# Performance work log

Measured on AMD Instinct MI355X. Metric: run time of the kernel, lower is better.

## Reference

```python
import jax, jax.numpy as jnp
import numpy as np

B, S, D, H = 2, 2048, 1024, 16
DK = D // H  # 64


def setup_inputs() -> dict:
    key = jax.random.key(0)
    ks = jax.random.split(key, 4)
    scale = 1.0 / np.sqrt(D)
    return {
        "q_input": jax.random.normal(ks[0], (B, S, D), dtype=jnp.float32),
        "W_q": jax.random.normal(ks[1], (D, D), dtype=jnp.float32) * scale,
        "b_q": jnp.zeros((D,), dtype=jnp.float32),
        "W_k": jax.random.normal(ks[2], (D, D), dtype=jnp.float32) * scale,
        "b_k": jnp.zeros((D,), dtype=jnp.float32),
        "W_v": jax.random.normal(ks[3], (D, D), dtype=jnp.float32) * scale,
        "b_v": jnp.zeros((D,), dtype=jnp.float32),
    }


def reference(q_input, W_q, b_q, W_k, b_k, W_v, b_v):
    # Self-attention: k_input and v_input default to q_input in the torch module.
    # nn.Linear computes x @ W.T + b
    q = q_input @ W_q.T + b_q
    k = q_input @ W_k.T + b_k
    v = q_input @ W_v.T + b_v

    # [B,S,D] -> [B,H,S,DK]
    def split_heads(x):
        return x.reshape(B, S, H, DK).transpose(0, 2, 1, 3)

    qh, kh, vh = split_heads(q), split_heads(k), split_heads(v)

    # scores [B,H,S,S]; causal mask added BEFORE scaling (as in source; -inf invariant)
    scores = jnp.einsum("bhqd,bhkd->bhqk", qh, kh)
    causal = jnp.tril(jnp.ones((S, S), dtype=bool))
    scores = jnp.where(causal[None, None], scores, -jnp.inf)
    scores = scores / jnp.sqrt(jnp.float32(DK))
    probs = jax.nn.softmax(scores, axis=-1)
    z = jnp.einsum("bhqk,bhkd->bhqd", probs, vh)  # [B,H,S,DK]
    # [B,H,S,DK] -> [B,S,H,DK] -> [B,S,D]
    return z.transpose(0, 2, 1, 3).reshape(B, S, D)
```

## Files before the change

### kernel.cpp

```cpp
#include <hip/hip_runtime.h>
#include <hip/hip_bf16.h>
#include <stdint.h>

typedef __attribute__((ext_vector_type(8))) short short8;
typedef __attribute__((ext_vector_type(4))) short short4v;
typedef __attribute__((ext_vector_type(4))) float f32x4;

#define B_ 2
#define S_ 2048
#define D_ 1024
#define H_ 16
#define DK_ 64
#define M_ (B_*S_)

#define WS_QKV   0
#define WS_XB    12582912
#define WS_WB    16777216

#define QSCALE (0.125f * 1.44269504088896f)

#define GLL16(g, l) __builtin_amdgcn_global_load_lds( \
    (const __attribute__((address_space(1))) void*)(g), \
    (__attribute__((address_space(3))) void*)(l), 16, 0, 0)

#define WAIT_VM0 asm volatile("s_waitcnt vmcnt(0)" ::: "memory")
#define WAIT_VM4 asm volatile("s_waitcnt vmcnt(4)" ::: "memory")
#define BARRIER_RAW asm volatile("s_barrier" ::: "memory")

static __device__ __forceinline__ short f2bf(float f){
  union { float f; unsigned u; } x; x.f = f;
  unsigned r = x.u + 0x7fff + ((x.u >> 16) & 1);
  return (short)(r >> 16);
}

__global__ __launch_bounds__(256) void cvt_bf16(
    const float* __restrict__ X,  const float* __restrict__ Wq,
    const float* __restrict__ Wk, const float* __restrict__ Wv,
    short* __restrict__ ws)
{
  const int z = blockIdx.z;
  const float* src; short* dst; int n;
  if (z == 0)      { src = X;  dst = ws + WS_XB;               n = M_*D_; }
  else if (z == 1) { src = Wq; dst = ws + WS_WB;               n = D_*D_; }
  else if (z == 2) { src = Wk; dst = ws + WS_WB + D_*D_;       n = D_*D_; }
  else             { src = Wv; dst = ws + WS_WB + 2*(D_*D_);   n = D_*D_; }
  const int stride = gridDim.x * blockDim.x * 4;
  for (int i = (blockIdx.x * blockDim.x + threadIdx.x) * 4; i < n; i += stride) {
    float4 v = *(const float4*)(src + i);
    short4v o;
    o.x = f2bf(v.x); o.y = f2bf(v.y); o.z = f2bf(v.z); o.w = f2bf(v.w);
    *(short4v*)(dst + i) = o;
  }
}

__global__ __launch_bounds__(256, 3) void qkv_gemm(
    const short* __restrict__ ws_in,
    const float* __restrict__ bq, const float* __restrict__ bk,
    const float* __restrict__ bv, short* __restrict__ qkv)
{
  const int z = blockIdx.z;
  const short* X  = ws_in + WS_XB;
  const short* Wm = ws_in + WS_WB + (size_t)z * (D_*D_);
  const float* bias = (z==0) ? bq : (z==1) ? bk : bv;
  short* out = qkv + (size_t)z * (M_*D_);

  __shared__ short lds[24576];

  const int t = threadIdx.x;
  const int w = t >> 6, lane = t & 63;
  const int quad = lane >> 4, l16 = lane & 15;
  const int wm = w & 1, wn = w >> 1;
  const int m0 = blockIdx.y * 128, n0 = blockIdx.x * 128;

  const int lr = lane >> 2, lc = lane & 3;
  const int csrc = lc ^ (lr & 3);
  const size_t arow0 = (size_t)(m0 + w*16     + lr) * D_ + csrc*8;
  const size_t arow1 = (size_t)(m0 + (w+4)*16 + lr) * D_ + csrc*8;
  const size_t brow0 = (size_t)(n0 + w*16     + lr) * D_ + csrc*8;
  const size_t brow1 = (size_t)(n0 + (w+4)*16 + lr) * D_ + csrc*8;

  f32x4 acc[4][4];
  #pragma unroll
  for (int i=0;i<4;i++)
    #pragma unroll
    for (int j=0;j<4;j++) acc[i][j] = (f32x4){0.f,0.f,0.f,0.f};

  #pragma unroll
  for (int p=0;p<2;p++){
    GLL16(X  + arow0 + p*32, lds + p*4096 + (w*16)*32);
    GLL16(X  + arow1 + p*32, lds + p*4096 + ((w+4)*16)*32);
    GLL16(Wm + brow0 + p*32, lds + 12288 + p*4096 + (w*16)*32);
    GLL16(Wm + brow1 + p*32, lds + 12288 + p*4096 + ((w+4)*16)*32);
  }

  const int ca = quad ^ (l16 & 3);
  int cur = 0;
  for (int kk = 0; kk < 32; kk++) {
    if (kk < 31) { WAIT_VM4; }
    else         { WAIT_VM0; }
    BARRIER_RAW;
    if (kk < 30) {
      int slot = cur + 2; if (slot >= 3) slot -= 3;
      const int ko = (kk+2)*32;
      short* An = lds + slot*4096;
      short* Bn = lds + 12288 + slot*4096;
      GLL16(X  + arow0 + ko, An + (w*16)*32);
      GLL16(X  + arow1 + ko, An + ((w+4)*16)*32);
      GLL16(Wm + brow0 + ko, Bn + (w*16)*32);
      GLL16(Wm + brow1 + ko, Bn + ((w+4)*16)*32);
    }
    const short* Ac = lds + cur*4096;
    const short* Bc = lds + 12288 + cur*4096;
    short8 af[4], bfr[4];
    #pragma unroll
    for (int mt=0;mt<4;mt++)
      af[mt] = *(const short8*)(Ac + (wm*64 + mt*16 + l16)*32 + ca*8);
    #pragma unroll
    for (int nt=0;nt<4;nt++)
      bfr[nt] = *(const short8*)(Bc + (wn*64 + nt*16 + l16)*32 + ca*8);
    if (z != 2) {
      #pragma unroll
      for (int mt=0;mt<4;mt++)
        #pragma unroll
        for (int nt=0;nt<4;nt++)
          acc[mt][nt] = __builtin_amdgcn_mfma_f32_16x16x32_bf16(af[mt], bfr[nt], acc[mt][nt], 0,0,0);
    } else {
      #pragma unroll
      for (int nt=0;nt<4;nt++)
        #pragma unroll
        for (int mt=0;mt<4;mt++)
          acc[nt][mt] = __builtin_amdgcn_mfma_f32_16x16x32_bf16(bfr[nt], af[mt], acc[nt][mt], 0,0,0);
    }
    cur = (cur==2) ? 0 : cur+1;
  }

  __syncthreads();

  if (z != 2) {
    const float scale = (z==0) ? QSCALE : 1.0f;
    #pragma unroll
    for (int nt=0;nt<4;nt++){
      const int col_l = wn*64 + nt*16 + l16;
      const float bvv = bias[n0 + col_l];
      #pragma unroll
      for (int mt=0;mt<4;mt++)
        #pragma unroll
        for (int i=0;i<4;i++){
          const int row_l = wm*64 + mt*16 + quad*4 + i;
          lds[row_l*136 + col_l] = f2bf((acc[mt][nt][i] + bvv) * scale);
        }
    }
    __syncthreads();
    #pragma unroll
    for (int k=0;k<8;k++){
      const int cid = k*256 + t;
      const int row = cid >> 4, cc = cid & 15;
      short8 vv = *(const short8*)(lds + row*136 + cc*8);
      const int m = m0 + row, bidx = m >> 11, s = m & 2047;
      const int n = n0 + cc*8, h = n >> 6, dd = n & 63;
      *(short8*)(out + (((size_t)(bidx*H_ + h))*S_ + s)*DK_ + dd) = vv;
    }
  } else {
    #pragma unroll
    for (int nt=0;nt<4;nt++)
      #pragma unroll
      for (int i=0;i<4;i++){
        const int n_l = wn*64 + nt*16 + quad*4 + i;
        const float bvv = bias[n0 + n_l];
        #pragma unroll
        for (int mt=0;mt<4;mt++){
          const int m_l = wm*64 + mt*16 + l16;
          lds[n_l*136 + m_l] = f2bf(acc[nt][mt][i] + bvv);
        }
      }
    __syncthreads();
    #pragma unroll
    for (int k=0;k<8;k++){
      const int cid = k*256 + t;
      const int rowN = cid >> 4, cc = cid & 15;
      short8 vv = *(const short8*)(lds + rowN*136 + cc*8);
      const int n = n0 + rowN, h = n >> 6, dd = n & 63;
      const int m = m0 + cc*8, bidx = m >> 11, s0 = m & 2047;
      *(short8*)(out + (((size_t)(bidx*H_ + h))*DK_ + dd)*S_ + s0) = vv;
    }
  }
}

__global__ __launch_bounds__(256, 3) void attn(
    const short* __restrict__ qkv, float* __restrict__ out)
{
  const int bh = blockIdx.y;
  const int qt = (gridDim.x - 1) - blockIdx.x;
  const short* Q  = qkv + (size_t)bh * (S_*DK_);
  const short* K  = Q + (size_t)(M_*D_);
  const short* VT = qkv + (size_t)(2*M_*D_) + (size_t)bh * (DK_*S_);

  __shared__ short Kbuf[2][4096];
  __shared__ short Vbuf[2][4096];
  __shared__ short Ps[8192];

  const int t = threadIdx.x;
  const int w = t >> 6, lane = t & 63;
  const int quad = lane >> 4, l16 = lane & 15;
  const int sw = l16 & 7;
  const int lr = lane >> 3, lc = lane & 7;
  const int csrc = lc ^ lr;

  short8 bq[2][2];
  #pragma unroll
  for (int kc=0;kc<2;kc++)
    #pragma unroll
    for (int mt=0;mt<2;mt++)
      bq[kc][mt] = *(const short8*)(Q + (size_t)(qt*128 + w*32 + mt*16 + l16)*DK_
                                      + (kc*4 + quad)*8);

  const int nkt = 2*qt + 2;
  #pragma unroll
  for (int j=0;j<2;j++){
    const int rb = (j*4 + w)*8;
    GLL16(K  + (size_t)(rb + lr)*DK_ + csrc*8, &Kbuf[0][0] + rb*64);
    GLL16(VT + (size_t)(rb + lr)*S_  + csrc*8, &Vbuf[0][0] + rb*64);
  }

  f32x4 o[2][4];
  float lsum[2];
  #pragma unroll
  for (int mt=0;mt<2;mt++){
    #pragma unroll
    for (int nd=0;nd<4;nd++) o[mt][nd] = (f32x4){0.f,0.f,0.f,0.f};
    lsum[mt] = 0.f;
  }

  const int pw_half = (quad & 1) * 4;
  const int pw_ckb  = quad >> 1;
  int cur = 0;

  for (int kt = 0; kt < nkt; kt++){
    WAIT_VM0;
    BARRIER_RAW;
    const int nxt = cur ^ 1;
    if (kt + 1 < nkt) {
      const int kb2 = (kt+1)*64;
      short* Kn = &Kbuf[nxt][0];
      short* Vn = &Vbuf[nxt][0];
      #pragma unroll
      for (int j=0;j<2;j++){
        const int rb = (j*4 + w)*8;
        GLL16(K  + (size_t)(kb2 + rb + lr)*DK_ + csrc*8, Kn + rb*64);
        GLL16(VT + (size_t)(rb + lr)*S_ + kb2 + csrc*8,  Vn + rb*64);
      }
    }
    const short* Kc = &Kbuf[cur][0];
    const short* Vc = &Vbuf[cur][0];
    const int kb = kt*64;

    f32x4 sc[4][2];
    #pragma unroll
    for (int ntk=0;ntk<4;ntk++)
      #pragma unroll
      for (int mt=0;mt<2;mt++) sc[ntk][mt] = (f32x4){0.f,0.f,0.f,0.f};
    #pragma unroll
    for (int kc=0;kc<2;kc++){
      const int xch = (kc*4 + quad) ^ sw;
      short8 ak[4];
      #pragma unroll
      for (int ntk=0;ntk<4;ntk++)
        ak[ntk] = *(const short8*)(Kc + (ntk*16 + l16)*64 + xch*8);
      #pragma unroll
      for (int ntk=0;ntk<4;ntk++)
        #pragma unroll
        for (int mt=0;mt<2;mt++)
          sc[ntk][mt] = __builtin_amdgcn_mfma_f32_16x16x32_bf16(ak[ntk], bq[kc][mt], sc[ntk][mt], 0,0,0);
    }

    const int q0w = qt*128 + w*32;
    if (kb + 63 > q0w) {
      #pragma unroll
      for (int ntk=0;ntk<4;ntk++)
        #pragma unroll
        for (int mt=0;mt<2;mt++){
          const int qg = q0w + mt*16 + l16;
          #pragma unroll
          for (int i=0;i<4;i++){
            const int kg = kb + ntk*16 + quad*4 + i;
            if (kg > qg) sc[ntk][mt][i] = -3.0e38f;
          }
        }
    }

    #pragma unroll
    for (int mt=0;mt<2;mt++){
      const int r = w*32 + mt*16 + l16;
      #pragma unroll
      for (int ntk=0;ntk<4;ntk++){
        float p0 = __builtin_amdgcn_exp2f(sc[ntk][mt][0]);
        float p1 = __builtin_amdgcn_exp2f(sc[ntk][mt][1]);
        float p2 = __builtin_amdgcn_exp2f(sc[ntk][mt][2]);
        float p3 = __builtin_amdgcn_exp2f(sc[ntk][mt][3]);
        lsum[mt] += (p0+p1) + (p2+p3);
        unsigned lo = __builtin_amdgcn_perm(__float_as_uint(p1), __float_as_uint(p0), 0x07060302u);
        unsigned hi = __builtin_amdgcn_perm(__float_as_uint(p3), __float_as_uint(p2), 0x07060302u);
        const int slot = (ntk*2 + pw_ckb) ^ sw;
        *(uint2*)(Ps + r*64 + slot*8 + pw_half) = make_uint2(lo, hi);
      }
    }
    asm volatile("" ::: "memory");

    #pragma unroll
    for (int kc=0;kc<2;kc++){
      const int xch = (kc*4 + quad) ^ sw;
      short8 pa[2], vb[4];
      #pragma unroll
      for (int mt=0;mt<2;mt++)
        pa[mt] = *(const short8*)(Ps + (w*32 + mt*16 + l16)*64 + xch*8);
      #pragma unroll
      for (int nd=0;nd<4;nd++)
        vb[nd] = *(const short8*)(Vc + (nd*16 + l16)*64 + xch*8);
      #pragma unroll
      for (int mt=0;mt<2;mt++)
        #pragma unroll
        for (int nd=0;nd<4;nd++)
          o[mt][nd] = __builtin_amdgcn_mfma_f32_16x16x32_bf16(pa[mt], vb[nd], o[mt][nd], 0,0,0);
    }
    cur = nxt;
  }

  const int bb = bh >> 4, h = bh & 15;
  float linv[2];
  #pragma unroll
  for (int mt=0;mt<2;mt++){
    float rs = lsum[mt];
    rs += __shfl_xor(rs, 16, 64);
    rs += __shfl_xor(rs, 32, 64);
    linv[mt] = 1.0f / rs;
  }
  #pragma unroll
  for (int mt=0;mt<2;mt++){
    #pragma unroll
    for (int i=0;i<4;i++){
      const float lw = __shfl(linv[mt], (quad<<4) + (quad<<2) + i, 64);
      const int q = qt*128 + w*32 + mt*16 + quad*4 + i;
      #pragma unroll
      for (int nd=0;nd<4;nd++){
        const int d = nd*16 + l16;
        out[ ((size_t)bb*S_ + q)*D_ + h*DK_ + d ] = o[mt][nd][i] * lw;
      }
    }
  }
}

extern "C" void kernel_launch(void* const* d_in, const int* in_sizes, int n_in,
                              void* d_out, int out_size, void* d_ws, size_t ws_size,
                              hipStream_t stream)
{
  (void)in_sizes; (void)n_in; (void)out_size; (void)ws_size;
  const float* X  = (const float*)d_in[0];
  const float* Wq = (const float*)d_in[1];
  const float* bq = (const float*)d_in[2];
  const float* Wk = (const float*)d_in[3];
  const float* bk = (const float*)d_in[4];
  const float* Wv = (const float*)d_in[5];
  const float* bv = (const float*)d_in[6];
  short* ws  = (short*)d_ws;
  float* out = (float*)d_out;

  dim3 g0(1024, 1, 4);
  cvt_bf16<<<g0, dim3(256,1,1), 0, stream>>>(X, Wq, Wk, Wv, ws);
  dim3 g1(D_/128, M_/128, 3);
  qkv_gemm<<<g1, dim3(256,1,1), 0, stream>>>(ws, bq, bk, bv, ws + WS_QKV);
  dim3 g2(S_/128, B_*H_);
  attn<<<g2, dim3(256,1,1), 0, stream>>>(ws + WS_QKV, out);
}
```

Baseline: 181.5 us.

## Enlarge QKV GEMM to 256x256 tiles with 8 waves and 4-stage LDS pipeline

The QKV projection GEMM moves from 128x128 tiles with 4 waves and a 3-slot buffer to 256x256 tiles with 8 waves, a 4-slot LDS ring, and a split-phase schedule that interleaves A/B global-to-LDS loads between two MFMA halves, raising s_setprio around the MFMA blocks. The aim is more data reuse per loaded byte and better overlap of loads with matrix math. The epilogue is rewritten to stage half the tile at a time through LDS. In exchange, the grid shrinks to 192 blocks, which may underfill the GPU's CUs, and register and LDS pressure per block rise.

```diff
diff --git a/kernel.cpp b/kernel.cpp
--- a/kernel.cpp
+++ b/kernel.cpp
@@ -25,6 +25,8 @@
 
 #define WAIT_VM0 asm volatile("s_waitcnt vmcnt(0)" ::: "memory")
 #define WAIT_VM4 asm volatile("s_waitcnt vmcnt(4)" ::: "memory")
+#define WAIT_VM8 asm volatile("s_waitcnt vmcnt(8)" ::: "memory")
+#define WAIT_LGKM0 asm volatile("s_waitcnt lgkmcnt(0)" ::: "memory")
 #define BARRIER_RAW asm volatile("s_barrier" ::: "memory")
 
 static __device__ __forceinline__ short f2bf(float f){
@@ -53,7 +55,7 @@
   }
 }
 
-__global__ __launch_bounds__(256, 3) void qkv_gemm(
+__global__ __launch_bounds__(512, 2) void qkv_gemm(
     const short* __restrict__ ws_in,
     const float* __restrict__ bq, const float* __restrict__ bk,
     const float* __restrict__ bv, short* __restrict__ qkv)
@@ -61,127 +63,157 @@
   const int z = blockIdx.z;
   const short* X  = ws_in + WS_XB;
   const short* Wm = ws_in + WS_WB + (size_t)z * (D_*D_);
-  const float* bias = (z==0) ? bq : (z==1) ? bk : bv;
   short* out = qkv + (size_t)z * (M_*D_);
 
-  __shared__ short lds[24576];
+  __shared__ __align__(16) short lds[65536];
 
   const int t = threadIdx.x;
   const int w = t >> 6, lane = t & 63;
   const int quad = lane >> 4, l16 = lane & 15;
-  const int wm = w & 1, wn = w >> 1;
-  const int m0 = blockIdx.y * 128, n0 = blockIdx.x * 128;
-
-  const int lr = lane >> 2, lc = lane & 3;
-  const int csrc = lc ^ (lr & 3);
-  const size_t arow0 = (size_t)(m0 + w*16     + lr) * D_ + csrc*8;
-  const size_t arow1 = (size_t)(m0 + (w+4)*16 + lr) * D_ + csrc*8;
-  const size_t brow0 = (size_t)(n0 + w*16     + lr) * D_ + csrc*8;
-  const size_t brow1 = (size_t)(n0 + (w+4)*16 + lr) * D_ + csrc*8;
-
-  f32x4 acc[4][4];
-  #pragma unroll
-  for (int i=0;i<4;i++)
+  const int wm = w >> 2, wn = w & 3;
+  const int m0 = blockIdx.y * 256, n0 = blockIdx.x * 256;
+
+  const int rl = t >> 2;
+  const int sl = (t & 3) ^ (rl & 3);
+  const short* sA0 = X  + (size_t)(m0 + rl) * D_ + sl*8;
+  const short* sA1 = sA0 + (size_t)128 * D_;
+  const short* sB0 = Wm + (size_t)(n0 + rl) * D_ + sl*8;
+  const short* sB1 = sB0 + (size_t)128 * D_;
+  const int ldsw = w << 9;
+
+  const int swz = quad ^ (l16 & 3);
+
+  f32x4 acc[8][4];
+  #pragma unroll
+  for (int i=0;i<8;i++)
     #pragma unroll
     for (int j=0;j<4;j++) acc[i][j] = (f32x4){0.f,0.f,0.f,0.f};
 
   #pragma unroll
-  for (int p=0;p<2;p++){
-    GLL16(X  + arow0 + p*32, lds + p*4096 + (w*16)*32);
-    GLL16(X  + arow1 + p*32, lds + p*4096 + ((w+4)*16)*32);
-    GLL16(Wm + brow0 + p*32, lds + 12288 + p*4096 + (w*16)*32);
-    GLL16(Wm + brow1 + p*32, lds + 12288 + p*4096 + ((w+4)*16)*32);
-  }
-
-  const int ca = quad ^ (l16 & 3);
-  int cur = 0;
-  for (int kk = 0; kk < 32; kk++) {
-    if (kk < 31) { WAIT_VM4; }
-    else         { WAIT_VM0; }
+  for (int p=0;p<3;p++){
+    GLL16(sA0 + p*32, lds + p*16384 + ldsw);
+    GLL16(sA1 + p*32, lds + p*16384 + 4096 + ldsw);
+    GLL16(sB0 + p*32, lds + p*16384 + 8192 + ldsw);
+    GLL16(sB1 + p*32, lds + p*16384 + 12288 + ldsw);
+  }
+  WAIT_VM8;
+  BARRIER_RAW;
+
+  for (int kt = 0; kt < 32; kt++) {
+    const int bf = kt & 3;
+    const short* bufA = lds + bf*16384;
+    const short* bufB = bufA + 8192;
+    const int tb = (kt + 3) & 3;
+    const int ko2 = (kt + 3) * 32;
+    const bool st = (kt + 3) < 32;
+
+    short8 aF[4], bF[4];
+    #pragma unroll
+    for (int mf=0; mf<4; mf++)
+      aF[mf] = *(const short8*)(bufA + (wm*128 + mf*16 + l16)*32 + swz*8);
+    #pragma unroll
+    for (int nf=0; nf<4; nf++)
+      bF[nf] = *(const short8*)(bufB + (wn*64 + nf*16 + l16)*32 + swz*8);
+    if (st) {
+      GLL16(sA0 + ko2, lds + tb*16384 + ldsw);
+      GLL16(sA1 + ko2, lds + tb*16384 + 4096 + ldsw);
+    }
     BARRIER_RAW;
-    if (kk < 30) {
-      int slot = cur + 2; if (slot >= 3) slot -= 3;
-      const int ko = (kk+2)*32;
-      short* An = lds + slot*4096;
-      short* Bn = lds + 12288 + slot*4096;
-      GLL16(X  + arow0 + ko, An + (w*16)*32);
-      GLL16(X  + arow1 + ko, An + ((w+4)*16)*32);
-      GLL16(Wm + brow0 + ko, Bn + (w*16)*32);
-      GLL16(Wm + brow1 + ko, Bn + ((w+4)*16)*32);
-    }
-    const short* Ac = lds + cur*4096;
-    const short* Bc = lds + 12288 + cur*4096;
-    short8 af[4], bfr[4];
-    #pragma unroll
-    for (int mt=0;mt<4;mt++)
-      af[mt] = *(const short8*)(Ac + (wm*64 + mt*16 + l16)*32 + ca*8);
-    #pragma unroll
-    for (int nt=0;nt<4;nt++)
-      bfr[nt] = *(const short8*)(Bc + (wn*64 + nt*16 + l16)*32 + ca*8);
-    if (z != 2) {
-      #pragma unroll
-      for (int mt=0;mt<4;mt++)
-        #pragma unroll
-        for (int nt=0;nt<4;nt++)
-          acc[mt][nt] = __builtin_amdgcn_mfma_f32_16x16x32_bf16(af[mt], bfr[nt], acc[mt][nt], 0,0,0);
-    } else {
-      #pragma unroll
-      for (int nt=0;nt<4;nt++)
-        #pragma unroll
-        for (int mt=0;mt<4;mt++)
-          acc[nt][mt] = __builtin_amdgcn_mfma_f32_16x16x32_bf16(bfr[nt], af[mt], acc[nt][mt], 0,0,0);
-    }
-    cur = (cur==2) ? 0 : cur+1;
+    WAIT_LGKM0;
+    __builtin_amdgcn_s_setprio(1);
+    #pragma unroll
+    for (int mf=0; mf<4; mf++)
+      #pragma unroll
+      for (int nf=0; nf<4; nf++)
+        acc[mf][nf] = __builtin_amdgcn_mfma_f32_16x16x32_bf16(aF[mf], bF[nf], acc[mf][nf], 0,0,0);
+    __builtin_amdgcn_s_setprio(0);
+    BARRIER_RAW;
+
+    #pragma unroll
+    for (int mf=0; mf<4; mf++)
+      aF[mf] = *(const short8*)(bufA + (wm*128 + 64 + mf*16 + l16)*32 + swz*8);
+    if (st) {
+      GLL16(sB0 + ko2, lds + tb*16384 + 8192 + ldsw);
+      GLL16(sB1 + ko2, lds + tb*16384 + 12288 + ldsw);
+    }
+    BARRIER_RAW;
+    WAIT_LGKM0;
+    __builtin_amdgcn_s_setprio(1);
+    #pragma unroll
+    for (int mf=0; mf<4; mf++)
+      #pragma unroll
+      for (int nf=0; nf<4; nf++)
+        acc[4+mf][nf] = __builtin_amdgcn_mfma_f32_16x16x32_bf16(aF[mf], bF[nf], acc[4+mf][nf], 0,0,0);
+    __builtin_amdgcn_s_setprio(0);
+    if      (kt < 29)  { WAIT_VM8; }
+    else if (kt == 29) { WAIT_VM4; }
+    else if (kt == 30) { WAIT_VM0; }
+    BARRIER_RAW;
   }
 
   __syncthreads();
 
   if (z != 2) {
     const float scale = (z==0) ? QSCALE : 1.0f;
-    #pragma unroll
-    for (int nt=0;nt<4;nt++){
-      const int col_l = wn*64 + nt*16 + l16;
-      const float bvv = bias[n0 + col_l];
-      #pragma unroll
-      for (int mt=0;mt<4;mt++)
+    const float* bias = (z==0) ? bq : bk;
+    float bv4[4];
+    #pragma unroll
+    for (int nf=0; nf<4; nf++) bv4[nf] = bias[n0 + wn*64 + nf*16 + l16];
+    short* ep = lds;
+    #pragma unroll
+    for (int p=0; p<2; p++){
+      if (wm == p){
         #pragma unroll
-        for (int i=0;i<4;i++){
-          const int row_l = wm*64 + mt*16 + quad*4 + i;
-          lds[row_l*136 + col_l] = f2bf((acc[mt][nt][i] + bvv) * scale);
-        }
-    }
-    __syncthreads();
-    #pragma unroll
-    for (int k=0;k<8;k++){
-      const int cid = k*256 + t;
-      const int row = cid >> 4, cc = cid & 15;
-      short8 vv = *(const short8*)(lds + row*136 + cc*8);
-      const int m = m0 + row, bidx = m >> 11, s = m & 2047;
-      const int n = n0 + cc*8, h = n >> 6, dd = n & 63;
-      *(short8*)(out + (((size_t)(bidx*H_ + h))*S_ + s)*DK_ + dd) = vv;
+        for (int mf=0; mf<8; mf++)
+          #pragma unroll
+          for (int nf=0; nf<4; nf++)
+            #pragma unroll
+            for (int i=0; i<4; i++)
+              ep[(mf*16 + quad*4 + i)*264 + wn*64 + nf*16 + l16] =
+                  f2bf((acc[mf][nf][i] + bv4[nf]) * scale);
+      }
+      __syncthreads();
+      #pragma unroll
+      for (int it=0; it<8; it++){
+        const int cid = it*512 + t;
+        const int row = cid >> 5, cc = cid & 31;
+        short8 vv = *(const short8*)(ep + row*264 + cc*8);
+        const int m = m0 + p*128 + row, bidx = m >> 11, s = m & 2047;
+        const int n = n0 + cc*8, h = n >> 6, dd = n & 63;
+        *(short8*)(out + (((size_t)(bidx*H_ + h))*S_ + s)*DK_ + dd) = vv;
+      }
+      __syncthreads();
     }
   } else {
-    #pragma unroll
-    for (int nt=0;nt<4;nt++)
-      #pragma unroll
-      for (int i=0;i<4;i++){
-        const int n_l = wn*64 + nt*16 + quad*4 + i;
-        const float bvv = bias[n0 + n_l];
+    float bv4[4];
+    #pragma unroll
+    for (int nf=0; nf<4; nf++) bv4[nf] = bv[n0 + wn*64 + nf*16 + l16];
+    short* ep = lds;
+    #pragma unroll
+    for (int p=0; p<2; p++){
+      if (wm == p){
         #pragma unroll
-        for (int mt=0;mt<4;mt++){
-          const int m_l = wm*64 + mt*16 + l16;
-          lds[n_l*136 + m_l] = f2bf(acc[nt][mt][i] + bvv);
-        }
-      }
-    __syncthreads();
-    #pragma unroll
-    for (int k=0;k<8;k++){
-      const int cid = k*256 + t;
-      const int rowN = cid >> 4, cc = cid & 15;
-      short8 vv = *(const short8*)(lds + rowN*136 + cc*8);
-      const int n = n0 + rowN, h = n >> 6, dd = n & 63;
-      const int m = m0 + cc*8, bidx = m >> 11, s0 = m & 2047;
-      *(short8*)(out + (((size_t)(bidx*H_ + h))*DK_ + dd)*S_ + s0) = vv;
+        for (int mf=0; mf<8; mf++)
+          #pragma unroll
+          for (int nf=0; nf<4; nf++)
+            #pragma unroll
+            for (int i=0; i<4; i++)
+              ep[(wn*64 + nf*16 + l16)*136 + mf*16 + quad*4 + i] =
+                  f2bf(acc[mf][nf][i] + bv4[nf]);
+      }
+      __syncthreads();
+      #pragma unroll
+      for (int it=0; it<8; it++){
+        const int cid = it*512 + t;
+        const int row = cid >> 4, cc = cid & 15;
+        short8 vv = *(const short8*)(ep + row*136 + cc*8);
+        const int n = n0 + row, h = n >> 6, dd = n & 63;
+        const int m0p = m0 + p*128;
+        const int bidx = m0p >> 11;
+        const int s = (m0p & 2047) + cc*8;
+        *(short8*)(out + (((size_t)(bidx*H_ + h))*DK_ + dd)*S_ + s) = vv;
+      }
+      __syncthreads();
     }
   }
 }
@@ -366,8 +398,8 @@
 
   dim3 g0(1024, 1, 4);
   cvt_bf16<<<g0, dim3(256,1,1), 0, stream>>>(X, Wq, Wk, Wv, ws);
-  dim3 g1(D_/128, M_/128, 3);
-  qkv_gemm<<<g1, dim3(256,1,1), 0, stream>>>(ws, bq, bk, bv, ws + WS_QKV);
+  dim3 g1(D_/256, M_/256, 3);
+  qkv_gemm<<<g1, dim3(512,1,1), 0, stream>>>(ws, bq, bk, bv, ws + WS_QKV);
   dim3 g2(S_/128, B_*H_);
   attn<<<g2, dim3(256,1,1), 0, stream>>>(ws + WS_QKV, out);
 }
```

Result: faster. 176.4 us (-2.8%).
